# Kernel tuning notes

Hardware: AMD Instinct MI355X
Metric: run time of the kernel (lower is better)

## Reference

```python
import jax, jax.numpy as jnp
import numpy as np

D_INNER = 1024
STATE = 16
DT_RANK = 64  # ceil(d_inner / 16)
LOG_EPS = -7.0
CLAMP = 20.0


def setup_inputs() -> dict:
    key = jax.random.key(0)
    ks = jax.random.split(key, 4)
    B, L = 2, 1024
    x = jax.random.normal(ks[0], (B, L, D_INNER), jnp.float32)
    # x_proj: Linear(d_inner -> dt_rank + 2*state_size, bias=False); stored as (in, out)
    W_xproj = jax.random.normal(ks[1], (D_INNER, DT_RANK + 2 * STATE), jnp.float32) * 0.02
    # dt_proj: Linear(dt_rank -> d_inner, bias=True)
    W_dt = jax.random.normal(ks[2], (DT_RANK, D_INNER), jnp.float32) * 0.02
    b_dt = jax.random.normal(ks[3], (D_INNER,), jnp.float32) * 0.02
    # A_log = log(arange(1..state_size)) repeated over d_inner rows
    A_log = jnp.log(jnp.tile(jnp.arange(1, STATE + 1, dtype=jnp.float32), (D_INNER, 1)))
    D = jnp.ones((D_INNER,), jnp.float32)
    return {"x": x, "W_xproj": W_xproj, "W_dt": W_dt, "b_dt": b_dt, "A_log": A_log, "D": D}


def reference(x, W_xproj, W_dt, b_dt, A_log, D):
    # x: (B, L, d_inner)
    proj = x @ W_xproj  # (B, L, dt_rank + 2*N)
    dt_inter = proj[..., :DT_RANK]
    B_ssm = proj[..., DT_RANK:DT_RANK + STATE]   # (B, L, N)
    C_ssm = proj[..., DT_RANK + STATE:]          # (B, L, N)

    delta = jax.nn.softplus(dt_inter @ W_dt + b_dt)  # (B, L, d_inner)

    # discretization (ZOH)
    A = -jnp.exp(A_log)  # (d_inner, N), negative
    log_delta_A = jnp.clip(delta[..., None] * A[None, None], LOG_EPS, CLAMP)
    delta_A = jnp.exp(log_delta_A)                              # (B, L, d, N)
    delta_B_u = (delta[..., None] * B_ssm[:, :, None, :]) * x[..., None]  # (B, L, d, N)

    # log-space cumsum scan
    log_dA = jnp.log(jnp.clip(delta_A, 1e-7, None))
    log_R = jnp.cumsum(log_dA, axis=1)
    R = jnp.exp(jnp.minimum(log_R, CLAMP))
    exp_neg_log_R = jnp.exp(jnp.minimum(-log_R, CLAMP))
    S = jnp.cumsum(delta_B_u * exp_neg_log_R, axis=1)
    h = R * S  # (B, L, d, N)

    y = jnp.einsum('bln,bldn->bld', C_ssm, h) + x * D
    return y
```

## Files before the change

kernel.cpp:

```cpp
#include <hip/hip_runtime.h>
#include <math.h>

#define D_INNER 1024
#define STATE   16
#define DT_RANK 64
#define NPROJ   96
#define LSEQ    1024
#define NBATCH  2

#define LOG2E   1.4426950408889634f
#define NEG7L2  (-7.0f * LOG2E)
#define P20L2   (20.0f * LOG2E)

template<int CTRL, int RMASK>
__device__ __forceinline__ float dppadd(float v) {
    int t = __builtin_amdgcn_update_dpp(0, __float_as_int(v), CTRL, RMASK, 0xf, false);
    return v + __int_as_float(t);
}
__device__ __forceinline__ float wave_iscan(float v) {
    v = dppadd<0x111, 0xf>(v);
    v = dppadd<0x112, 0xf>(v);
    v = dppadd<0x114, 0xf>(v);
    v = dppadd<0x118, 0xf>(v);
    v = dppadd<0x142, 0xa>(v);
    v = dppadd<0x143, 0xc>(v);
    return v;
}

__global__ __launch_bounds__(768) void proj_kernel(
        const float* __restrict__ x, const float* __restrict__ Wx,
        float* __restrict__ projdt, float* __restrict__ Bg, float* __restrict__ Cg) {
    const int tid = threadIdx.x;
    const int j  = tid % 96;
    const int kq = tid / 96;
    const int row0 = blockIdx.x * 8;

    __shared__ float xs[8 * 1024];
    __shared__ float red[8][8][96];

    {
        const float4* src = (const float4*)(x + (size_t)row0 * 1024);
        #pragma unroll
        for (int i = 0; i < 3; ++i) {
            int idx = tid + 768 * i;
            if (idx < 2048) {
                float4 v = src[idx];
                *(float4*)&xs[idx * 4] = v;
            }
        }
    }
    __syncthreads();

    const float* wp = Wx + (size_t)(kq * 128) * 96 + j;
    const float* xk = &xs[kq * 128];

    float a[8];
    #pragma unroll
    for (int r = 0; r < 8; ++r) a[r] = 0.f;

    #pragma unroll 8
    for (int k = 0; k < 128; ++k) {
        float w = wp[(size_t)k * 96];
        #pragma unroll
        for (int r = 0; r < 8; ++r)
            a[r] = fmaf(xk[r * 1024 + k], w, a[r]);
    }

    #pragma unroll
    for (int r = 0; r < 8; ++r) red[kq][r][j] = a[r];
    __syncthreads();

    {
        const int r  = tid / 96;
        const int jj = tid % 96;
        float s = 0.f;
        #pragma unroll
        for (int p = 0; p < 8; ++p) s += red[p][r][jj];
        const int row = row0 + r;
        const int b = row >> 10, l = row & 1023;
        if (jj < 64)      projdt[(size_t)row * 64 + jj] = s;
        else if (jj < 80) Bg[((size_t)b * 16 + (jj - 64)) * 1024 + l] = s;
        else              Cg[((size_t)b * 16 + (jj - 80)) * 1024 + l] = s;
    }
}

__global__ __launch_bounds__(256) void delta_kernel(
        const float* __restrict__ projdt, const float* __restrict__ Wdt,
        const float* __restrict__ bdt, const float* __restrict__ x,
        float* __restrict__ delta_t, float* __restrict__ u_t) {
    const int bid = blockIdx.x;
    const int lt = bid >> 4;
    const int dt = bid & 15;
    const int row0 = lt * 64;
    const int d0 = dt * 64;
    const int tid = threadIdx.x;

    __shared__ float pl[64][69];
    __shared__ float wlbuf[64 * 68];
    __shared__ float dtile[64][65];
    float (*wl)[68] = (float(*)[68])wlbuf;

    {
        const float4* src = (const float4*)(projdt + (size_t)row0 * 64);
        #pragma unroll
        for (int i = 0; i < 4; ++i) {
            int f4i = tid + 256 * i;
            float4 v = src[f4i];
            int l = f4i >> 4, k4 = (f4i & 15) << 2;
            pl[l][k4+0] = v.x; pl[l][k4+1] = v.y; pl[l][k4+2] = v.z; pl[l][k4+3] = v.w;
        }
    }
    {
        #pragma unroll
        for (int i = 0; i < 4; ++i) {
            int f4i = tid + 256 * i;
            int k = f4i >> 4, m4 = (f4i & 15) << 2;
            float4 v = *(const float4*)(Wdt + (size_t)k * 1024 + d0 + m4);
            *(float4*)&wl[k][m4] = v;
        }
    }
    __syncthreads();

    const int lsub = tid & 63;
    const int dq = tid >> 6;
    float acc[16];
    #pragma unroll
    for (int i = 0; i < 16; ++i) acc[i] = 0.f;

    #pragma unroll 4
    for (int k = 0; k < 64; ++k) {
        float p = pl[lsub][k];
        const float4* wr = (const float4*)&wl[k][dq * 16];
        float4 w0 = wr[0], w1 = wr[1], w2 = wr[2], w3 = wr[3];
        acc[0]  = fmaf(p, w0.x, acc[0]);  acc[1]  = fmaf(p, w0.y, acc[1]);
        acc[2]  = fmaf(p, w0.z, acc[2]);  acc[3]  = fmaf(p, w0.w, acc[3]);
        acc[4]  = fmaf(p, w1.x, acc[4]);  acc[5]  = fmaf(p, w1.y, acc[5]);
        acc[6]  = fmaf(p, w1.z, acc[6]);  acc[7]  = fmaf(p, w1.w, acc[7]);
        acc[8]  = fmaf(p, w2.x, acc[8]);  acc[9]  = fmaf(p, w2.y, acc[9]);
        acc[10] = fmaf(p, w2.z, acc[10]); acc[11] = fmaf(p, w2.w, acc[11]);
        acc[12] = fmaf(p, w3.x, acc[12]); acc[13] = fmaf(p, w3.y, acc[13]);
        acc[14] = fmaf(p, w3.z, acc[14]); acc[15] = fmaf(p, w3.w, acc[15]);
    }

    #pragma unroll
    for (int i = 0; i < 16; ++i) {
        float v = acc[i] + bdt[d0 + dq * 16 + i];
        float sp = fmaxf(v, 0.f) + log1pf(__expf(-fabsf(v)));
        dtile[dq * 16 + i][lsub] = sp;
    }
    __syncthreads();

    float (*xs)[65] = (float(*)[65])wlbuf;
    {
        #pragma unroll
        for (int i = 0; i < 4; ++i) {
            int f4i = tid + 256 * i;
            int l = f4i >> 4, m4 = (f4i & 15) << 2;
            float4 v = *(const float4*)(x + (size_t)(row0 + l) * 1024 + d0 + m4);
            xs[l][m4+0] = v.x; xs[l][m4+1] = v.y; xs[l][m4+2] = v.z; xs[l][m4+3] = v.w;
        }
    }
    __syncthreads();

    {
        int dp_ = tid >> 2, seg = tid & 3;
        int b = row0 >> 10, l0 = row0 & 1023;
        size_t off = ((size_t)b * 1024 + d0 + dp_) * 1024 + l0 + seg * 16;
        float* ddst = delta_t + off;
        float* udst = u_t + off;
        #pragma unroll
        for (int m = 0; m < 4; ++m) {
            int lb = seg * 16 + m * 4;
            float4 v;
            v.x = dtile[dp_][lb + 0];
            v.y = dtile[dp_][lb + 1];
            v.z = dtile[dp_][lb + 2];
            v.w = dtile[dp_][lb + 3];
            float4 u;
            u.x = v.x * xs[lb + 0][dp_];
            u.y = v.y * xs[lb + 1][dp_];
            u.z = v.z * xs[lb + 2][dp_];
            u.w = v.w * xs[lb + 3][dp_];
            ((float4*)ddst)[m] = v;
            ((float4*)udst)[m] = u;
        }
    }
}

__global__ __launch_bounds__(256) void scan_kernel(
        const float* __restrict__ delta_t, const float* __restrict__ u_t,
        const float* __restrict__ Bg, const float* __restrict__ Cg,
        const float* __restrict__ A_log, const float* __restrict__ Dvec,
        float* __restrict__ yout) {
    const int bid0 = blockIdx.x;
    const int bid  = (bid0 & 7) * 64 + (bid0 >> 3);
    const int w    = threadIdx.x >> 6;
    const int lane = threadIdx.x & 63;
    const int chain = bid * 4 + w;
    const int b = chain >> 10;
    const int d = chain & 1023;
    const int l0 = lane * 16;

    __shared__ float T[4][1088];

    const size_t choff = ((size_t)b * 1024 + d) * 1024 + l0;

    float dl[16], ul[16];
    #pragma unroll
    for (int k = 0; k < 4; ++k) {
        float4 v = *(const float4*)(delta_t + choff + k * 4);
        dl[4*k+0] = v.x; dl[4*k+1] = v.y; dl[4*k+2] = v.z; dl[4*k+3] = v.w;
    }
    #pragma unroll
    for (int k = 0; k < 4; ++k) {
        float4 v = *(const float4*)(u_t + choff + k * 4);
        ul[4*k+0] = v.x; ul[4*k+1] = v.y; ul[4*k+2] = v.z; ul[4*k+3] = v.w;
    }

    const float* Bp = Bg + (size_t)b * 16 * 1024 + l0;
    const float* Cp = Cg + (size_t)b * 16 * 1024 + l0;
    const float Dd = Dvec[d];

    float y[16];
    #pragma unroll
    for (int l = 0; l < 16; ++l)
        y[l] = ul[l] * __builtin_amdgcn_rcpf(dl[l]) * Dd;

    float Bc[16], Cc[16];
    #pragma unroll
    for (int k = 0; k < 4; ++k) {
        float4 bv = *(const float4*)(Bp + k * 4);
        Bc[4*k+0] = bv.x; Bc[4*k+1] = bv.y; Bc[4*k+2] = bv.z; Bc[4*k+3] = bv.w;
        float4 cv = *(const float4*)(Cp + k * 4);
        Cc[4*k+0] = cv.x; Cc[4*k+1] = cv.y; Cc[4*k+2] = cv.z; Cc[4*k+3] = cv.w;
    }

    #pragma unroll 1
    for (int n = 0; n < 16; ++n) {
        const int np = (n < 15) ? n + 1 : 15;
        float Bn[16], Cn[16];
        #pragma unroll
        for (int k = 0; k < 4; ++k) {
            float4 bv = *(const float4*)(Bp + (size_t)np * 1024 + k * 4);
            Bn[4*k+0] = bv.x; Bn[4*k+1] = bv.y; Bn[4*k+2] = bv.z; Bn[4*k+3] = bv.w;
            float4 cv = *(const float4*)(Cp + (size_t)np * 1024 + k * 4);
            Cn[4*k+0] = cv.x; Cn[4*k+1] = cv.y; Cn[4*k+2] = cv.z; Cn[4*k+3] = cv.w;
        }

        const float a = -__expf(A_log[d * 16 + n]) * LOG2E;

        float local = 0.f;
        #pragma unroll
        for (int l = 0; l < 16; ++l)
            local += fmaxf(dl[l] * a, NEG7L2);
        float incl = wave_iscan(local);
        float c = incl - local;

        float g[16];
        float srun = 0.f;
        #pragma unroll
        for (int l = 0; l < 16; ++l) {
            c += fmaxf(dl[l] * a, NEG7L2);
            g[l] = Cc[l] * exp2f(c);
            srun = fmaf(ul[l] * Bc[l], exp2f(fminf(-c, P20L2)), srun);
            y[l] = fmaf(g[l], srun, y[l]);
        }

        float incl2 = wave_iscan(srun);
        float lex = incl2 - srun;
        #pragma unroll
        for (int l = 0; l < 16; ++l)
            y[l] = fmaf(g[l], lex, y[l]);

        #pragma unroll
        for (int l = 0; l < 16; ++l) { Bc[l] = Bn[l]; Cc[l] = Cn[l]; }
    }

    #pragma unroll
    for (int k = 0; k < 16; ++k) {
        int l = l0 + k;
        T[w][l + (l >> 4)] = y[k];
    }
    __syncthreads();

    {
        const int d0 = (bid * 4) & 1023;
        float* yb = yout + (size_t)b * 1024 * 1024 + d0;
        const int t = threadIdx.x;
        #pragma unroll
        for (int m = 0; m < 4; ++m) {
            int l = t * 4 + m;
            int sw = l + (l >> 4);
            float4 o = make_float4(T[0][sw], T[1][sw], T[2][sw], T[3][sw]);
            *(float4*)(yb + (size_t)l * 1024) = o;
        }
    }
}

extern "C" void kernel_launch(void* const* d_in, const int* in_sizes, int n_in,
                              void* d_out, int out_size, void* d_ws, size_t ws_size,
                              hipStream_t stream) {
    const float* x    = (const float*)d_in[0];
    const float* Wx   = (const float*)d_in[1];
    const float* Wdt  = (const float*)d_in[2];
    const float* bdt  = (const float*)d_in[3];
    const float* Alog = (const float*)d_in[4];
    const float* Dvec = (const float*)d_in[5];
    float* y = (float*)d_out;

    float* projdt  = (float*)d_ws;
    float* Bgp     = projdt + (size_t)2048 * 64;
    float* Cgp     = Bgp + (size_t)2 * 16 * 1024;
    float* delta_t = Cgp + (size_t)2 * 16 * 1024;
    float* u_t     = delta_t + (size_t)2 * 1024 * 1024;

    proj_kernel<<<256, 768, 0, stream>>>(x, Wx, projdt, Bgp, Cgp);
    delta_kernel<<<512, 256, 0, stream>>>(projdt, Wdt, bdt, x, delta_t, u_t);
    scan_kernel<<<512, 256, 0, stream>>>(delta_t, u_t, Bgp, Cgp, Alog, Dvec, y);
}
```

Baseline: 71.51 us.

## Split scan state dimension across two waves per chain and combine via LDS

The scan kernel now uses two waves per (batch, channel) chain, each handling 8 of the 16 state entries, so blocks grow to 512 threads. The partial outputs are summed through a new shared-memory buffer before the transposed store. This doubles the number of resident waves to hide the latency of the serial per-state loop. The cost is duplicated delta/u loads and per-wave prefix sums over delta, an extra barrier, and the loss of the B/C register prefetch pipelining.

```diff
diff --git a/kernel.cpp b/kernel.cpp
--- a/kernel.cpp
+++ b/kernel.cpp
@@ -187,20 +187,23 @@
     }
 }
 
-__global__ __launch_bounds__(256) void scan_kernel(
+__global__ __launch_bounds__(512, 4) void scan_kernel(
         const float* __restrict__ delta_t, const float* __restrict__ u_t,
         const float* __restrict__ Bg, const float* __restrict__ Cg,
         const float* __restrict__ A_log, const float* __restrict__ Dvec,
         float* __restrict__ yout) {
     const int bid0 = blockIdx.x;
     const int bid  = (bid0 & 7) * 64 + (bid0 >> 3);
-    const int w    = threadIdx.x >> 6;
+    const int wv   = threadIdx.x >> 6;
+    const int ch   = wv >> 1;
+    const int half = wv & 1;
     const int lane = threadIdx.x & 63;
-    const int chain = bid * 4 + w;
+    const int chain = bid * 4 + ch;
     const int b = chain >> 10;
     const int d = chain & 1023;
     const int l0 = lane * 16;
 
+    __shared__ float ycomb[4][64][17];
     __shared__ float T[4][1088];
 
     const size_t choff = ((size_t)b * 1024 + d) * 1024 + l0;
@@ -219,34 +222,21 @@
 
     const float* Bp = Bg + (size_t)b * 16 * 1024 + l0;
     const float* Cp = Cg + (size_t)b * 16 * 1024 + l0;
-    const float Dd = Dvec[d];
 
     float y[16];
-    #pragma unroll
-    for (int l = 0; l < 16; ++l)
-        y[l] = ul[l] * __builtin_amdgcn_rcpf(dl[l]) * Dd;
-
-    float Bc[16], Cc[16];
-    #pragma unroll
-    for (int k = 0; k < 4; ++k) {
-        float4 bv = *(const float4*)(Bp + k * 4);
-        Bc[4*k+0] = bv.x; Bc[4*k+1] = bv.y; Bc[4*k+2] = bv.z; Bc[4*k+3] = bv.w;
-        float4 cv = *(const float4*)(Cp + k * 4);
-        Cc[4*k+0] = cv.x; Cc[4*k+1] = cv.y; Cc[4*k+2] = cv.z; Cc[4*k+3] = cv.w;
+    if (half == 0) {
+        const float Dd = Dvec[d];
+        #pragma unroll
+        for (int l = 0; l < 16; ++l)
+            y[l] = ul[l] * __builtin_amdgcn_rcpf(dl[l]) * Dd;
+    } else {
+        #pragma unroll
+        for (int l = 0; l < 16; ++l) y[l] = 0.f;
     }
 
     #pragma unroll 1
-    for (int n = 0; n < 16; ++n) {
-        const int np = (n < 15) ? n + 1 : 15;
-        float Bn[16], Cn[16];
-        #pragma unroll
-        for (int k = 0; k < 4; ++k) {
-            float4 bv = *(const float4*)(Bp + (size_t)np * 1024 + k * 4);
-            Bn[4*k+0] = bv.x; Bn[4*k+1] = bv.y; Bn[4*k+2] = bv.z; Bn[4*k+3] = bv.w;
-            float4 cv = *(const float4*)(Cp + (size_t)np * 1024 + k * 4);
-            Cn[4*k+0] = cv.x; Cn[4*k+1] = cv.y; Cn[4*k+2] = cv.z; Cn[4*k+3] = cv.w;
-        }
-
+    for (int jn = 0; jn < 8; ++jn) {
+        const int n = half * 8 + jn;
         const float a = -__expf(A_log[d * 16 + n]) * LOG2E;
 
         float local = 0.f;
@@ -256,13 +246,22 @@
         float incl = wave_iscan(local);
         float c = incl - local;
 
+        float Bv[16], Cv[16];
+        #pragma unroll
+        for (int k = 0; k < 4; ++k) {
+            float4 bv = *(const float4*)(Bp + (size_t)n * 1024 + k * 4);
+            Bv[4*k+0] = bv.x; Bv[4*k+1] = bv.y; Bv[4*k+2] = bv.z; Bv[4*k+3] = bv.w;
+            float4 cv = *(const float4*)(Cp + (size_t)n * 1024 + k * 4);
+            Cv[4*k+0] = cv.x; Cv[4*k+1] = cv.y; Cv[4*k+2] = cv.z; Cv[4*k+3] = cv.w;
+        }
+
         float g[16];
         float srun = 0.f;
         #pragma unroll
         for (int l = 0; l < 16; ++l) {
             c += fmaxf(dl[l] * a, NEG7L2);
-            g[l] = Cc[l] * exp2f(c);
-            srun = fmaf(ul[l] * Bc[l], exp2f(fminf(-c, P20L2)), srun);
+            g[l] = Cv[l] * exp2f(c);
+            srun = fmaf(ul[l] * Bv[l], exp2f(fminf(-c, P20L2)), srun);
             y[l] = fmaf(g[l], srun, y[l]);
         }
 
@@ -271,25 +270,29 @@
         #pragma unroll
         for (int l = 0; l < 16; ++l)
             y[l] = fmaf(g[l], lex, y[l]);
-
-        #pragma unroll
-        for (int l = 0; l < 16; ++l) { Bc[l] = Bn[l]; Cc[l] = Cn[l]; }
-    }
-
-    #pragma unroll
-    for (int k = 0; k < 16; ++k) {
-        int l = l0 + k;
-        T[w][l + (l >> 4)] = y[k];
+    }
+
+    if (half == 1) {
+        #pragma unroll
+        for (int l = 0; l < 16; ++l)
+            ycomb[ch][lane][l] = y[l];
+    }
+    __syncthreads();
+    if (half == 0) {
+        #pragma unroll
+        for (int k = 0; k < 16; ++k) {
+            int l = l0 + k;
+            T[ch][l + (l >> 4)] = y[k] + ycomb[ch][lane][k];
+        }
     }
     __syncthreads();
 
     {
         const int d0 = (bid * 4) & 1023;
         float* yb = yout + (size_t)b * 1024 * 1024 + d0;
-        const int t = threadIdx.x;
-        #pragma unroll
-        for (int m = 0; m < 4; ++m) {
-            int l = t * 4 + m;
+        #pragma unroll
+        for (int m = 0; m < 2; ++m) {
+            int l = threadIdx.x * 2 + m;
             int sw = l + (l >> 4);
             float4 o = make_float4(T[0][sw], T[1][sw], T[2][sw], T[3][sw]);
             *(float4*)(yb + (size_t)l * 1024) = o;
@@ -316,5 +319,5 @@
 
     proj_kernel<<<256, 768, 0, stream>>>(x, Wx, projdt, Bgp, Cgp);
     delta_kernel<<<512, 256, 0, stream>>>(projdt, Wdt, bdt, x, delta_t, u_t);
-    scan_kernel<<<512, 256, 0, stream>>>(delta_t, u_t, Bgp, Cgp, Alog, Dvec, y);
-}
+    scan_kernel<<<512, 512, 0, stream>>>(delta_t, u_t, Bgp, Cgp, Alog, Dvec, y);
+}
```

Measured after the change: 70.35 us. No clear change (-1.6%).
